# Performance work log

Hardware: AMD Instinct MI355X
Metric: run time of the kernel (lower is better)

The kernel has to match this reference:

```python
import jax, jax.numpy as jnp
import numpy as np

EPS_NORM = 1e-12
BN_EPS = 1e-5
TEMP = 0.07


def _l2norm(x, axis):
    n = jnp.sqrt(jnp.sum(x * x, axis=axis, keepdims=True))
    return x / jnp.maximum(n, EPS_NORM)


def _bn_eval(z, w, b):
    # inference-mode BatchNorm2d with running_mean=0, running_var=1
    s = w / jnp.sqrt(jnp.asarray(1.0 + BN_EPS, z.dtype))
    return z * s[None, :, None, None] + b[None, :, None, None]


def setup_inputs() -> dict:
    key = jax.random.key(0)
    ks = jax.random.split(key, 8)
    B, C, H, W = 16, 256, 64, 64
    KD, P = 128, 256
    x = jax.random.normal(ks[0], (B, C, H, W), jnp.float32)
    m_features = jax.random.normal(ks[1], (P, KD), jnp.float32)
    q_w = jax.random.normal(ks[2], (KD, C), jnp.float32) * 0.05
    k_w = jax.random.normal(ks[3], (KD, KD), jnp.float32) * 0.05
    v_w = jax.random.normal(ks[4], (KD, KD), jnp.float32) * 0.05
    o_w = jax.random.normal(ks[5], (C, KD), jnp.float32) * 0.05
    dw_w = jax.random.normal(ks[6], (C, 1, 3, 3), jnp.float32) * 0.1
    return {
        "x": x, "m_features": m_features,
        "q_w": q_w, "q_b": jnp.zeros((KD,), jnp.float32),
        "k_w": k_w, "k_b": jnp.zeros((KD,), jnp.float32),
        "v_w": v_w, "v_b": jnp.zeros((KD,), jnp.float32),
        "o_w": o_w, "o_b": jnp.zeros((C,), jnp.float32),
        "dw_w": dw_w,
        "bn1_w": jnp.ones((C,), jnp.float32), "bn1_b": jnp.zeros((C,), jnp.float32),
        "bn2_w": jnp.ones((C,), jnp.float32), "bn2_b": jnp.zeros((C,), jnp.float32),
        "gamma": jnp.ones((C,), jnp.float32) * 1e-5,
    }


def reference(x, m_features, q_w, q_b, k_w, k_b, v_w, v_b, o_w, o_b,
              dw_w, bn1_w, bn1_b, bn2_w, bn2_b, gamma):
    B, C, H, W = x.shape
    KD = q_w.shape[0]
    residual = x
    # q_proj 1x1 conv -> [B,KD,H,W], L2-normalize over channel dim
    q = jnp.einsum('bchw,kc->bkhw', x, q_w) + q_b[None, :, None, None]
    q = _l2norm(q, axis=1)
    q = q.reshape(B, KD, H * W).transpose(0, 2, 1)  # [B, HW, KD]
    # k/v projections of memory bank [P, KD]
    k = _l2norm(m_features @ k_w.T + k_b, axis=-1)
    v = m_features @ v_w.T + v_b
    # fp32 attention with clamped logits
    q32, k32, v32 = q.astype(jnp.float32), k.astype(jnp.float32), v.astype(jnp.float32)
    logits = jnp.clip(jnp.einsum('bnd,pd->bnp', q32, k32) / TEMP, -30.0, 30.0)
    attn = jax.nn.softmax(logits, axis=-1)
    out = jnp.einsum('bnp,pd->bnd', attn, v32).astype(x.dtype)
    out = out.transpose(0, 2, 1).reshape(B, KD, H, W)
    # out_proj 1x1 conv -> [B,C,H,W]
    out = jnp.einsum('bkhw,ck->bchw', out, o_w) + o_b[None, :, None, None]
    # local branch: depthwise 3x3 conv + BN + exact GELU
    local = jax.lax.conv_general_dilated(
        out, dw_w, window_strides=(1, 1), padding='SAME',
        feature_group_count=C,
        dimension_numbers=('NCHW', 'OIHW', 'NCHW'))
    local = jax.nn.gelu(_bn_eval(local, bn1_w, bn1_b), approximate=False)
    out = out + local
    return _bn_eval(residual + out * gamma[None, :, None, None], bn2_w, bn2_b)
```

## Files before the change

### kernel.cpp

```cpp
#include <hip/hip_runtime.h>
#include <hip/hip_bf16.h>
#include <math.h>

#define B_ 16
#define C_ 256
#define H_ 64
#define W_ 64
#define KD_ 128
#define P_ 256
#define HW_ (H_ * W_)

typedef __bf16 bf16;
typedef bf16 bf16x8_t __attribute__((ext_vector_type(8)));
typedef float f32x4_t __attribute__((ext_vector_type(4)));
typedef float f32x16_t __attribute__((ext_vector_type(16)));
typedef unsigned char u8;

__device__ __forceinline__ unsigned cvt_pk_fp8_lo(float a, float b, unsigned old) {
#if __has_builtin(__builtin_amdgcn_cvt_pk_fp8_f32)
    return __builtin_amdgcn_cvt_pk_fp8_f32(a, b, old, false);
#else
    unsigned r = old;
    asm("v_cvt_pk_fp8_f32 %0, %1, %2" : "+v"(r) : "v"(a), "v"(b));
    return r;
#endif
}
__device__ __forceinline__ unsigned cvt_pk_fp8_hi(float a, float b, unsigned old) {
#if __has_builtin(__builtin_amdgcn_cvt_pk_fp8_f32)
    return __builtin_amdgcn_cvt_pk_fp8_f32(a, b, old, true);
#else
    unsigned r = old;
    asm("v_cvt_pk_fp8_f32 %0, %1, %2 op_sel:[0,0,1]" : "+v"(r) : "v"(a), "v"(b));
    return r;
#endif
}
__device__ __forceinline__ uint2 pack8_fp8(const float* f) {
    uint2 r;
    r.x = cvt_pk_fp8_hi(f[2], f[3], cvt_pk_fp8_lo(f[0], f[1], 0u));
    r.y = cvt_pk_fp8_hi(f[6], f[7], cvt_pk_fp8_lo(f[4], f[5], 0u));
    return r;
}

__global__ __launch_bounds__(128) void k_prep1(
    const float* __restrict__ m_feat,
    const float* __restrict__ k_w, const float* __restrict__ k_b,
    const float* __restrict__ v_w, const float* __restrict__ v_b,
    float* __restrict__ kn_f, float* __restrict__ v_f)
{
    const int p = blockIdx.x;
    const int j = threadIdx.x;
    __shared__ float msh[KD_];
    __shared__ float red[2];
    msh[j] = m_feat[p * KD_ + j];
    __syncthreads();

    float ka = k_b[j];
    float va = v_b[j];
#pragma unroll 4
    for (int d = 0; d < KD_; ++d) {
        const float m = msh[d];
        ka = fmaf(m, k_w[j * KD_ + d], ka);
        va = fmaf(m, v_w[j * KD_ + d], va);
    }
    float s = ka * ka;
#pragma unroll
    for (int o = 1; o < 64; o <<= 1) s += __shfl_xor(s, o);
    if ((j & 63) == 0) red[j >> 6] = s;
    __syncthreads();
    s = red[0] + red[1];
    const float inv = 1.0f / (0.07f * fmaxf(sqrtf(s), 1e-12f));
    kn_f[p * KD_ + j] = ka * inv;
    v_f[p * KD_ + j] = va;
}

__global__ __launch_bounds__(256) void k_prep23(
    const float* __restrict__ o_w, const float* __restrict__ v_f,
    const float* __restrict__ q_w, const float* __restrict__ kn_f,
    u8* __restrict__ m28, u8* __restrict__ qw8, u8* __restrict__ kn8)
{
    if (blockIdx.x < 256) {
        const int c = blockIdx.x;
        const int p = threadIdx.x;
        __shared__ float osh[KD_];
        if (p < KD_) osh[p] = o_w[c * KD_ + p];
        __syncthreads();
        float acc = 0.f;
#pragma unroll 4
        for (int k = 0; k < KD_; ++k) acc = fmaf(osh[k], v_f[p * KD_ + k], acc);
        const int mt = c >> 5, r = c & 31;
        const int ks = p >> 4, sub = (p >> 3) & 1, jj = p & 7;
        const unsigned pk = cvt_pk_fp8_lo(acc * 16.0f, 0.f, 0u);
        m28[(((mt * 16 + ks) * 64) + sub * 32 + r) * 8 + jj] = (u8)(pk & 0xffu);
    } else {
        const int t = (blockIdx.x - 256) * 256 + threadIdx.x;
        float f[8];
        if (t < 4096) {
            const int lane = t & 63, g = t >> 6, mt = g >> 4, ks = g & 15;
            const int row = mt * 32 + (lane & 31), k0 = ks * 16 + (lane >> 5) * 8;
            const float* src = q_w + row * C_ + k0;
#pragma unroll
            for (int j = 0; j < 8; ++j) f[j] = src[j] * 16.0f;
            ((uint2*)qw8)[t] = pack8_fp8(f);
        } else {
            const int u = t - 4096;
            const int lane = u & 63, g = u >> 6, mt = g >> 3, ks = g & 7;
            const int row = mt * 32 + (lane & 31), k0 = ks * 16 + (lane >> 5) * 8;
            const float* src = kn_f + row * KD_ + k0;
#pragma unroll
            for (int j = 0; j < 8; ++j) f[j] = src[j];
            ((uint2*)kn8)[u] = pack8_fp8(f);
        }
    }
}

__global__ __launch_bounds__(512, 8) void k_attn(
    const float* __restrict__ x,
    const float* __restrict__ q_b, const float* __restrict__ o_b,
    const u8* __restrict__ qw8, const u8* __restrict__ kn8,
    const u8* __restrict__ m28, bf16* __restrict__ outf)
{
    __shared__ __align__(16) char lds[29696];
    char* const xs   = lds;
    char* const qbuf = lds + 16384;
    char* const ebuf = lds;
    float* const ss_lds   = (float*)(lds + 24576);
    float* const pmax_lds = (float*)(lds + 25600);
    float* const sum_lds  = (float*)(lds + 27648);

    const int h = blockIdx.x;
    const int b = blockIdx.y;
    const int tid = threadIdx.x;
    const int lane = tid & 63;
    const int wid = tid >> 6;
    const int l31 = lane & 31;
    const int kh  = lane >> 5;

    {
        const int wq = tid & 15;
        const int cg = tid >> 4;
        const int c0 = cg * 8;
        const float* xrow = x + (size_t)b * C_ * HW_ + h * W_ + wq * 4;
        float v[8][4];
#pragma unroll
        for (int jj = 0; jj < 8; ++jj) {
            const f32x4_t t = *(const f32x4_t*)(xrow + (size_t)(c0 + jj) * HW_);
            v[jj][0] = t[0]; v[jj][1] = t[1]; v[jj][2] = t[2]; v[jj][3] = t[3];
        }
#pragma unroll
        for (int k = 0; k < 4; ++k) {
            const int pix = wq * 4 + k;
            float f[8];
#pragma unroll
            for (int jj = 0; jj < 8; ++jj) f[jj] = v[jj][k];
            *(uint2*)(xs + pix * 256 + (c0 ^ ((pix & 31) << 3))) = pack8_fp8(f);
        }
    }
    __syncthreads();

    const int mtA = wid & 3, nhalf = wid >> 2;
    {
        f32x16_t qacc;
#pragma unroll
        for (int i = 0; i < 16; ++i) qacc[i] = 0.f;
        const int pix = nhalf * 32 + l31;
#pragma unroll
        for (int ks = 0; ks < 16; ++ks) {
            const long a = *(const long*)(qw8 + ((mtA * 16 + ks) * 64 + lane) * 8);
            const long bx = *(const long*)(xs + pix * 256 + ((ks * 16 + kh * 8) ^ (l31 << 3)));
            qacc = __builtin_amdgcn_mfma_f32_32x32x16_fp8_fp8(a, bx, qacc, 0, 0, 0);
        }
        float ssp = 0.f;
#pragma unroll
        for (int g = 0; g < 4; ++g) {
            const f32x4_t qbv = *(const f32x4_t*)(q_b + mtA * 32 + g * 8 + kh * 4);
#pragma unroll
            for (int i = 0; i < 4; ++i) {
                const float qv = qacc[g * 4 + i] + 16.0f * qbv[i];
                qacc[g * 4 + i] = qv;
                ssp = fmaf(qv, qv, ssp);
            }
        }
        ssp += __shfl_xor(ssp, 32);
        if (lane < 32) ss_lds[pix * 4 + mtA] = ssp;
#pragma unroll
        for (int g = 0; g < 4; ++g) {
            const unsigned qw_ = cvt_pk_fp8_hi(qacc[g * 4 + 2], qacc[g * 4 + 3],
                                 cvt_pk_fp8_lo(qacc[g * 4 + 0], qacc[g * 4 + 1], 0u));
            *(unsigned*)(qbuf + pix * 128 +
                         ((mtA * 32 + g * 8 + kh * 4) ^ ((l31 & 15) << 3))) = qw_;
        }
    }
    __syncthreads();

    f32x16_t lacc0, lacc1;
#pragma unroll
    for (int i = 0; i < 16; ++i) { lacc0[i] = 0.f; lacc1[i] = 0.f; }
#pragma unroll
    for (int ks = 0; ks < 8; ++ks) {
        const long a = *(const long*)(kn8 + ((wid * 8 + ks) * 64 + lane) * 8);
        const long bq0 = *(const long*)(qbuf + (0 * 32 + l31) * 128 +
                                        ((ks * 16 + kh * 8) ^ ((l31 & 15) << 3)));
        const long bq1 = *(const long*)(qbuf + (1 * 32 + l31) * 128 +
                                        ((ks * 16 + kh * 8) ^ ((l31 & 15) << 3)));
        lacc0 = __builtin_amdgcn_mfma_f32_32x32x16_fp8_fp8(a, bq0, lacc0, 0, 0, 0);
        lacc1 = __builtin_amdgcn_mfma_f32_32x32x16_fp8_fp8(a, bq1, lacc1, 0, 0, 0);
    }
#pragma unroll
    for (int nt = 0; nt < 2; ++nt) {
        const int pix = nt * 32 + l31;
        float mx;
        if (nt == 0) {
            mx = lacc0[0];
#pragma unroll
            for (int i = 1; i < 16; ++i) mx = fmaxf(mx, lacc0[i]);
        } else {
            mx = lacc1[0];
#pragma unroll
            for (int i = 1; i < 16; ++i) mx = fmaxf(mx, lacc1[i]);
        }
        mx = fmaxf(mx, __shfl_xor(mx, 32));
        if (lane < 32) pmax_lds[pix * 8 + wid] = mx;
    }
    __syncthreads();

#pragma unroll
    for (int nt = 0; nt < 2; ++nt) {
        const int pix = nt * 32 + l31;
        const f32x4_t s4 = *(const f32x4_t*)(ss_lds + pix * 4);
        const float qinv = 1.0f / fmaxf(sqrtf(s4[0] + s4[1] + s4[2] + s4[3]), 1e-12f);
        const f32x4_t ma = *(const f32x4_t*)(pmax_lds + pix * 8);
        const f32x4_t mb = *(const f32x4_t*)(pmax_lds + pix * 8 + 4);
        const float cof = 5.545177444479562f -
                          fmaxf(fmaxf(fmaxf(ma[0], ma[1]), fmaxf(ma[2], ma[3])),
                                fmaxf(fmaxf(mb[0], mb[1]), fmaxf(mb[2], mb[3]))) * qinv;
        float sm = 0.f;
#pragma unroll
        for (int g = 0; g < 4; ++g) {
            float e[4];
#pragma unroll
            for (int i = 0; i < 4; ++i) {
                const float lv = (nt == 0) ? lacc0[g * 4 + i] : lacc1[g * 4 + i];
                e[i] = __expf(fmaf(lv, qinv, cof));
                sm += e[i];
            }
            const unsigned ew = cvt_pk_fp8_hi(e[2], e[3],
                                cvt_pk_fp8_lo(e[0], e[1], 0u));
            const int p0 = wid * 32 + g * 8 + kh * 4;
            *(unsigned*)(ebuf + pix * 256 + (p0 ^ (l31 << 3))) = ew;
        }
        sm += __shfl_xor(sm, 32);
        if (lane < 32) sum_lds[pix * 8 + wid] = sm;
    }
    __syncthreads();

    f32x16_t oacc0, oacc1;
#pragma unroll
    for (int i = 0; i < 16; ++i) { oacc0[i] = 0.f; oacc1[i] = 0.f; }
#pragma unroll
    for (int ks = 0; ks < 16; ++ks) {
        const long a = *(const long*)(m28 + ((wid * 16 + ks) * 64 + lane) * 8);
        const long be0 = *(const long*)(ebuf + (0 * 32 + l31) * 256 +
                                        ((ks * 16 + kh * 8) ^ (l31 << 3)));
        const long be1 = *(const long*)(ebuf + (1 * 32 + l31) * 256 +
                                        ((ks * 16 + kh * 8) ^ (l31 << 3)));
        oacc0 = __builtin_amdgcn_mfma_f32_32x32x16_fp8_fp8(a, be0, oacc0, 0, 0, 0);
        oacc1 = __builtin_amdgcn_mfma_f32_32x32x16_fp8_fp8(a, be1, oacc1, 0, 0, 0);
    }
    {
        const f32x4_t sa0 = *(const f32x4_t*)(sum_lds + (0 * 32 + l31) * 8);
        const f32x4_t sb0 = *(const f32x4_t*)(sum_lds + (0 * 32 + l31) * 8 + 4);
        const f32x4_t sa1 = *(const f32x4_t*)(sum_lds + (1 * 32 + l31) * 8);
        const f32x4_t sb1 = *(const f32x4_t*)(sum_lds + (1 * 32 + l31) * 8 + 4);
        const float rs0 = 1.0f / (16.0f * (sa0[0] + sa0[1] + sa0[2] + sa0[3] +
                                           sb0[0] + sb0[1] + sb0[2] + sb0[3]));
        const float rs1 = 1.0f / (16.0f * (sa1[0] + sa1[1] + sa1[2] + sa1[3] +
                                           sb1[0] + sb1[1] + sb1[2] + sb1[3]));
        bf16* const obase = outf + (size_t)b * C_ * HW_ + h * W_;
#pragma unroll
        for (int g = 0; g < 4; ++g) {
            const f32x4_t obv = *(const f32x4_t*)(o_b + wid * 32 + g * 8 + kh * 4);
#pragma unroll
            for (int i = 0; i < 4; ++i) {
                const int c = wid * 32 + g * 8 + kh * 4 + i;
                obase[(size_t)c * HW_ + l31]      = (bf16)fmaf(oacc0[g * 4 + i], rs0, obv[i]);
                obase[(size_t)c * HW_ + 32 + l31] = (bf16)fmaf(oacc1[g * 4 + i], rs1, obv[i]);
            }
        }
    }
}

__global__ __launch_bounds__(256) void k_post(
    const float* __restrict__ x, const bf16* __restrict__ outf,
    const float* __restrict__ dw_w,
    const float* __restrict__ bn1_w, const float* __restrict__ bn1_b,
    const float* __restrict__ bn2_w, const float* __restrict__ bn2_b,
    const float* __restrict__ gamma, float* __restrict__ y)
{
    __shared__ __align__(16) bf16 os[HW_];
    const int bc = blockIdx.x;
    const int c = bc & (C_ - 1);
    const int tid = threadIdx.x;

    const bf16* oc = outf + (size_t)bc * HW_;
#pragma unroll
    for (int it = 0; it < 2; ++it) {
        const int e = (it * 256 + tid) * 8;
        *(bf16x8_t*)&os[e] = *(const bf16x8_t*)&oc[e];
    }

    const float cbn = 0.99999500003750f;
    const float s1 = bn1_w[c] * cbn, b1 = bn1_b[c];
    const float s2 = bn2_w[c] * cbn, b2 = bn2_b[c];
    const float g = gamma[c];
    float kw[9];
#pragma unroll
    for (int j = 0; j < 9; ++j) kw[j] = dw_w[c * 9 + j];

    __syncthreads();

    const int w = tid & 63;
    const int h0 = (tid >> 6) * 16;

    float r0[3], r1[3], r2[3];
    auto ldrow = [&](int hh, float* r) {
        if ((unsigned)hh < (unsigned)H_) {
            r[1] = (float)os[hh * W_ + w];
            r[0] = (w > 0) ? (float)os[hh * W_ + w - 1] : 0.f;
            r[2] = (w < W_ - 1) ? (float)os[hh * W_ + w + 1] : 0.f;
        } else {
            r[0] = r[1] = r[2] = 0.f;
        }
    };
    ldrow(h0 - 1, r0);
    ldrow(h0, r1);

    const float* xc = x + (size_t)bc * HW_;
    float* yc = y + (size_t)bc * HW_;

#pragma unroll
    for (int i = 0; i < 16; ++i) {
        const int h = h0 + i;
        ldrow(h + 1, r2);
        float conv = kw[0] * r0[0];
        conv = fmaf(kw[1], r0[1], conv);
        conv = fmaf(kw[2], r0[2], conv);
        conv = fmaf(kw[3], r1[0], conv);
        conv = fmaf(kw[4], r1[1], conv);
        conv = fmaf(kw[5], r1[2], conv);
        conv = fmaf(kw[6], r2[0], conv);
        conv = fmaf(kw[7], r2[1], conv);
        conv = fmaf(kw[8], r2[2], conv);
        const float center = r1[1];
        const float t = fmaf(conv, s1, b1);
        const float lg = t / (1.0f + __expf(-1.702f * t));
        const int idx = h * W_ + w;
        yc[idx] = fmaf(center + lg, g, xc[idx]) * s2 + b2;
#pragma unroll
        for (int j = 0; j < 3; ++j) { r0[j] = r1[j]; r1[j] = r2[j]; }
    }
}

extern "C" void kernel_launch(void* const* d_in, const int* in_sizes, int n_in,
                              void* d_out, int out_size, void* d_ws, size_t ws_size,
                              hipStream_t stream)
{
    const float* x     = (const float*)d_in[0];
    const float* m_f   = (const float*)d_in[1];
    const float* q_w   = (const float*)d_in[2];
    const float* q_b   = (const float*)d_in[3];
    const float* k_w   = (const float*)d_in[4];
    const float* k_b   = (const float*)d_in[5];
    const float* v_w   = (const float*)d_in[6];
    const float* v_b   = (const float*)d_in[7];
    const float* o_w   = (const float*)d_in[8];
    const float* o_b   = (const float*)d_in[9];
    const float* dw_w  = (const float*)d_in[10];
    const float* bn1_w = (const float*)d_in[11];
    const float* bn1_b = (const float*)d_in[12];
    const float* bn2_w = (const float*)d_in[13];
    const float* bn2_b = (const float*)d_in[14];
    const float* gamma = (const float*)d_in[15];

    char* ws = (char*)d_ws;
    u8*    qw8   = (u8*)(ws);
    u8*    kn8   = (u8*)(ws + (32 << 10));
    u8*    m28   = (u8*)(ws + (64 << 10));
    bf16*  outf  = (bf16*)(ws + (384 << 10));
    float* kn_f  = (float*)(ws + (384 << 10));
    float* v_f   = (float*)(ws + (384 << 10) + (128 << 10));

    k_prep1<<<dim3(P_), dim3(128), 0, stream>>>(m_f, k_w, k_b, v_w, v_b,
                                                kn_f, v_f);
    k_prep23<<<dim3(288), dim3(256), 0, stream>>>(o_w, v_f, q_w, kn_f,
                                                  m28, qw8, kn8);
    k_attn<<<dim3(H_, B_), dim3(512), 0, stream>>>(x, q_b, o_b, qw8, kn8,
                                                   m28, outf);
    k_post<<<dim3(B_ * C_), dim3(256), 0, stream>>>(
        x, outf, dw_w, bn1_w, bn1_b, bn2_w, bn2_b, gamma, (float*)d_out);
}
```

Before: 76.30 us.

## Pre-transpose x into an fp8 MFMA-ready layout in a separate kernel

Adds a k_xpose kernel that converts x to fp8 and writes it in a per-row, channel-blocked layout matching the MFMA B-operand fragment. k_attn then reads those fragments straight from global memory instead of staging and swizzling x through LDS. This drops a barrier and the in-kernel conversion from the attention kernel. In exchange it adds a kernel launch and an extra pass that reads all of x and writes an fp8 copy to a larger workspace.

```diff
diff --git a/kernel.cpp b/kernel.cpp
--- a/kernel.cpp
+++ b/kernel.cpp
@@ -39,6 +39,44 @@
     r.x = cvt_pk_fp8_hi(f[2], f[3], cvt_pk_fp8_lo(f[0], f[1], 0u));
     r.y = cvt_pk_fp8_hi(f[6], f[7], cvt_pk_fp8_lo(f[4], f[5], 0u));
     return r;
+}
+
+__global__ __launch_bounds__(512, 8) void k_xpose(
+    const float* __restrict__ x, u8* __restrict__ x8)
+{
+    __shared__ __align__(16) u8 tile[16 * 2048];
+    const int cblk = blockIdx.x >> 1;
+    const int ph   = blockIdx.x & 1;
+    const int b    = blockIdx.y;
+    const int t = threadIdx.x;
+
+    {
+        const int cl = t >> 5, sub = t & 31;
+        const float* src = x + ((size_t)b * C_ + cblk * 16 + cl) * HW_ + ph * 2048;
+#pragma unroll
+        for (int i = 0; i < 16; ++i) {
+            const f32x4_t v = *(const f32x4_t*)(src + (i * 32 + sub) * 4);
+            const unsigned w = cvt_pk_fp8_hi(v[2], v[3],
+                               cvt_pk_fp8_lo(v[0], v[1], 0u));
+            *(unsigned*)&tile[cl * 2048 + (i * 32 + sub) * 4] = w;
+        }
+    }
+    __syncthreads();
+
+    {
+        const int pr = t & 63;
+        const int r0 = t >> 6;
+#pragma unroll
+        for (int it = 0; it < 4; ++it) {
+            const int r = it * 8 + r0;
+            const int lp = r * 64 + pr;
+            union { u8 bytes[16]; uint4 u; } g;
+#pragma unroll
+            for (int c = 0; c < 16; ++c) g.bytes[c] = tile[c * 2048 + lp];
+            const int h = ph * 32 + r;
+            *(uint4*)(x8 + (((size_t)(b * 64 + h) * 16 + cblk) << 10) + pr * 16) = g.u;
+        }
+    }
 }
 
 __global__ __launch_bounds__(128) void k_prep1(
@@ -114,15 +152,14 @@
 }
 
 __global__ __launch_bounds__(512, 8) void k_attn(
-    const float* __restrict__ x,
+    const u8* __restrict__ x8,
     const float* __restrict__ q_b, const float* __restrict__ o_b,
     const u8* __restrict__ qw8, const u8* __restrict__ kn8,
     const u8* __restrict__ m28, bf16* __restrict__ outf)
 {
     __shared__ __align__(16) char lds[29696];
-    char* const xs   = lds;
+    char* const ebuf = lds;
     char* const qbuf = lds + 16384;
-    char* const ebuf = lds;
     float* const ss_lds   = (float*)(lds + 24576);
     float* const pmax_lds = (float*)(lds + 25600);
     float* const sum_lds  = (float*)(lds + 27648);
@@ -135,30 +172,9 @@
     const int l31 = lane & 31;
     const int kh  = lane >> 5;
 
-    {
-        const int wq = tid & 15;
-        const int cg = tid >> 4;
-        const int c0 = cg * 8;
-        const float* xrow = x + (size_t)b * C_ * HW_ + h * W_ + wq * 4;
-        float v[8][4];
-#pragma unroll
-        for (int jj = 0; jj < 8; ++jj) {
-            const f32x4_t t = *(const f32x4_t*)(xrow + (size_t)(c0 + jj) * HW_);
-            v[jj][0] = t[0]; v[jj][1] = t[1]; v[jj][2] = t[2]; v[jj][3] = t[3];
-        }
-#pragma unroll
-        for (int k = 0; k < 4; ++k) {
-            const int pix = wq * 4 + k;
-            float f[8];
-#pragma unroll
-            for (int jj = 0; jj < 8; ++jj) f[jj] = v[jj][k];
-            *(uint2*)(xs + pix * 256 + (c0 ^ ((pix & 31) << 3))) = pack8_fp8(f);
-        }
-    }
-    __syncthreads();
-
     const int mtA = wid & 3, nhalf = wid >> 2;
     {
+        const u8* xrow = x8 + ((size_t)(b * 64 + h) << 14);
         f32x16_t qacc;
 #pragma unroll
         for (int i = 0; i < 16; ++i) qacc[i] = 0.f;
@@ -166,7 +182,7 @@
 #pragma unroll
         for (int ks = 0; ks < 16; ++ks) {
             const long a = *(const long*)(qw8 + ((mtA * 16 + ks) * 64 + lane) * 8);
-            const long bx = *(const long*)(xs + pix * 256 + ((ks * 16 + kh * 8) ^ (l31 << 3)));
+            const long bx = *(const long*)(xrow + ks * 1024 + pix * 16 + kh * 8);
             qacc = __builtin_amdgcn_mfma_f32_32x32x16_fp8_fp8(a, bx, qacc, 0, 0, 0);
         }
         float ssp = 0.f;
@@ -385,15 +401,17 @@
     u8*    qw8   = (u8*)(ws);
     u8*    kn8   = (u8*)(ws + (32 << 10));
     u8*    m28   = (u8*)(ws + (64 << 10));
-    bf16*  outf  = (bf16*)(ws + (384 << 10));
-    float* kn_f  = (float*)(ws + (384 << 10));
-    float* v_f   = (float*)(ws + (384 << 10) + (128 << 10));
-
+    u8*    x8    = (u8*)(ws + (1 << 20));
+    bf16*  outf  = (bf16*)(ws + (17 << 20));
+    float* kn_f  = (float*)(ws + (17 << 20));
+    float* v_f   = (float*)(ws + (17 << 20) + (128 << 10));
+
+    k_xpose<<<dim3(32, B_), dim3(512), 0, stream>>>(x, x8);
     k_prep1<<<dim3(P_), dim3(128), 0, stream>>>(m_f, k_w, k_b, v_w, v_b,
                                                 kn_f, v_f);
     k_prep23<<<dim3(288), dim3(256), 0, stream>>>(o_w, v_f, q_w, kn_f,
                                                   m28, qw8, kn8);
-    k_attn<<<dim3(H_, B_), dim3(512), 0, stream>>>(x, q_b, o_b, qw8, kn8,
+    k_attn<<<dim3(H_, B_), dim3(512), 0, stream>>>(x8, q_b, o_b, qw8, kn8,
                                                    m28, outf);
     k_post<<<dim3(B_ * C_), dim3(256), 0, stream>>>(
         x, outf, dw_w, bn1_w, bn1_b, bn2_w, bn2_b, gamma, (float*)d_out);
```

Result: slower. 87.09 us (+14.1%).
